# Optimization experiments

Hardware: AMD Instinct MI355X
Metric: run time of the kernel (lower is better)

## Reference

```python
import jax, jax.numpy as jnp
import numpy as np
import math

NH, NKV, D = 32, 8, 128  # heads, kv heads, head dim

def _alibi_slopes(n):
    cp2 = 2 ** math.floor(math.log2(n))
    base = 2.0 ** (-8.0 / cp2)
    slopes = base ** np.arange(1, cp2 + 1, dtype=np.float32)
    if cp2 != n:
        extra_base = 2.0 ** (-4.0 / cp2)
        extra = extra_base ** np.arange(1, 1 + 2 * (n - cp2), 2, dtype=np.float32)
        slopes = np.concatenate([slopes, extra])
    return slopes.astype(np.float32)

def setup_inputs() -> dict:
    key = jax.random.key(0)
    k1, k2, k3 = jax.random.split(key, 3)
    B, S, H = 4, 1024, 4096
    qkv_out = NH * D + 2 * NKV * D  # 6144
    return {
        "hidden_states": jax.random.normal(k1, (B, S, H), jnp.float32) * 0.02,
        "w_qkv": jax.random.normal(k2, (H, qkv_out), jnp.float32) * 0.02,
        "w_o": jax.random.normal(k3, (NH * D, H), jnp.float32) * 0.02,
    }

def reference(hidden_states, w_qkv, w_o):
    B, S, H = hidden_states.shape
    G = NH // NKV  # query groups per kv head
    scale = D ** -0.5

    qkv = hidden_states @ w_qkv  # [B,S,6144]
    q = qkv[..., : NH * D].reshape(B, S, NKV, G, D)
    k = qkv[..., NH * D : NH * D + NKV * D].reshape(B, S, NKV, D)
    v = qkv[..., NH * D + NKV * D :].reshape(B, S, NKV, D)

    scores = jnp.einsum("bqhgd,bkhd->bhgqk", q, k) * scale  # [B,NKV,G,S,S]

    slopes = jnp.asarray(_alibi_slopes(NH)).reshape(NKV, G)  # head order
    pos = jnp.arange(S)
    rel = pos[:, None] - pos[None, :]  # i - j
    sqrt_dist = jnp.sqrt(jnp.maximum(rel, 0).astype(jnp.float32))
    bias = -slopes[:, :, None, None] * sqrt_dist  # ALiBi-sqrt bias
    bias = jnp.where(rel[None, None] >= 0, bias, -jnp.inf)  # causal mask

    attn = jax.nn.softmax(scores + bias[None], axis=-1)
    out = jnp.einsum("bhgqk,bkhd->bqhgd", attn, v).reshape(B, S, NH * D)
    return out @ w_o
```

## Files before the change

kernel.cpp:

```cpp
#include <hip/hip_runtime.h>
#include <stdint.h>

typedef __attribute__((ext_vector_type(4))) float floatx4;
typedef __attribute__((ext_vector_type(8))) short short8;
typedef unsigned short ushort_t;

#define DEVI __device__ __forceinline__

constexpr int Bc   = 4;
constexpr int Sc   = 1024;
constexpr int Hc   = 4096;
constexpr int NHc  = 32;
constexpr int NKVc = 8;
constexpr int Dc   = 128;
constexpr int QKVO = 6144;
constexpr int Mc   = Bc * Sc;

DEVI ushort_t f2bf(float f) {
  union { float f; unsigned u; } x; x.f = f;
  unsigned u = x.u;
  u += 0x7fffu + ((u >> 16) & 1u);
  return (ushort_t)(u >> 16);
}

DEVI short8 cvt8(floatx4 a, floatx4 b) {
  short8 r;
  r[0] = (short)f2bf(a[0]); r[1] = (short)f2bf(a[1]);
  r[2] = (short)f2bf(a[2]); r[3] = (short)f2bf(a[3]);
  r[4] = (short)f2bf(b[0]); r[5] = (short)f2bf(b[1]);
  r[6] = (short)f2bf(b[2]); r[7] = (short)f2bf(b[3]);
  return r;
}

DEVI void load_lds16(const ushort_t* g, ushort_t* l) {
  __builtin_amdgcn_global_load_lds(
      (const __attribute__((address_space(1))) void*)g,
      (__attribute__((address_space(3))) void*)l, 16, 0, 0);
}

#define BARRIER()  asm volatile("s_barrier" ::: "memory")
#define LGKM0()    asm volatile("s_waitcnt lgkmcnt(0)" ::: "memory")
#define VMCNT(n)   asm volatile("s_waitcnt vmcnt(" #n ")" ::: "memory")

__global__ __launch_bounds__(256)
void cvt_bf16(const float* __restrict__ src, ushort_t* __restrict__ dst, int n8)
{
  const int i = blockIdx.x * 256 + threadIdx.x;
  if (i >= n8) return;
  const floatx4 f0 = *(const floatx4*)(src + (size_t)i * 8);
  const floatx4 f1 = *(const floatx4*)(src + (size_t)i * 8 + 4);
  *(short8*)(dst + (size_t)i * 8) = cvt8(f0, f1);
}

__global__ __launch_bounds__(256)
void transpose_cvt(const float* __restrict__ src, ushort_t* __restrict__ dst,
                   int R, int C)
{
  __shared__ float ts[64][67];
  const int cb = C >> 6;
  const int r0 = (blockIdx.x / cb) << 6;
  const int c0 = (blockIdx.x % cb) << 6;
  const int t  = threadIdx.x;

  const int lr = t >> 4, lc = (t & 15) << 2;
#pragma unroll
  for (int i = 0; i < 4; ++i) {
    const floatx4 v = *(const floatx4*)(src + (size_t)(r0 + lr + 16 * i) * C + c0 + lc);
#pragma unroll
    for (int j = 0; j < 4; ++j) ts[lr + 16 * i][lc + j] = v[j];
  }
  __syncthreads();

  const int c     = ((t >> 6) << 4) + ((t & 63) >> 2);
  const int chunk = t & 3;
  short8 t0, t1;
#pragma unroll
  for (int k = 0; k < 8; ++k) t0[k] = (short)f2bf(ts[chunk * 16 + k][c]);
#pragma unroll
  for (int k = 0; k < 8; ++k) t1[k] = (short)f2bf(ts[chunk * 16 + 8 + k][c]);
  ushort_t* dp = dst + (size_t)(c0 + c) * R + r0 + chunk * 16;
  *(short8*)dp       = t0;
  *(short8*)(dp + 8) = t1;
}

__global__ __launch_bounds__(256)
void v_transpose(const ushort_t* __restrict__ qkv, ushort_t* __restrict__ vt)
{
  __shared__ ushort_t ts[64][72];
  const int bid = blockIdx.x;
  const int db  = bid & 1;
  const int sb  = (bid >> 1) & 15;
  const int hkv = (bid >> 5) & 7;
  const int b   = bid >> 8;
  const int t   = threadIdx.x;

  const ushort_t* src = qkv + (size_t)(b * Sc + sb * 64) * QKVO
                        + (NHc * Dc + NKVc * Dc) + hkv * Dc + db * 64;
  const int lr = t >> 3, lc = (t & 7) * 8;
  *(short8*)&ts[lr][lc]      = *(const short8*)(src + (size_t)lr * QKVO + lc);
  *(short8*)&ts[lr + 32][lc] = *(const short8*)(src + (size_t)(lr + 32) * QKVO + lc);
  __syncthreads();

  ushort_t* dst = vt + ((size_t)(b * NKVc + hkv) * Dc + db * 64) * Sc + sb * 64;
  const int dr  = t >> 2;
  const int sc0 = (t & 3) * 16;
  short8 o0, o1;
#pragma unroll
  for (int k = 0; k < 8; ++k) o0[k] = (short)ts[sc0 + k][dr];
#pragma unroll
  for (int k = 0; k < 8; ++k) o1[k] = (short)ts[sc0 + 8 + k][dr];
  *(short8*)(dst + (size_t)dr * Sc + sc0)     = o0;
  *(short8*)(dst + (size_t)dr * Sc + sc0 + 8) = o1;
}

template<bool OBF16>
__global__ __launch_bounds__(512, 2)
void gemm_nt8(const ushort_t* __restrict__ A, const ushort_t* __restrict__ BT,
              void* __restrict__ Cp, int M, int N, int K)
{
  __shared__ __align__(16) ushort_t As[2][256 * 64];
  __shared__ __align__(16) ushort_t Bs[2][256 * 64];

  const int nb  = N >> 8;
  const int nwg = (M >> 8) * nb;
  int bid = blockIdx.x;
  bid = (bid & 7) * (nwg >> 3) + (bid >> 3);
  const int bm = bid / nb, bn = bid % nb;
  const int m0 = bm << 8, n0 = bn << 8;

  const int tid  = threadIdx.x;
  const int wid  = tid >> 6, lane = tid & 63;
  const int wm   = wid >> 2, wn = wid & 3;
  const int fr   = lane & 15;
  const int g16  = (lane >> 4) << 4;
  const int rsw  = (fr & 7) << 4;
  const int l8   = lane >> 3;
  const int scol = ((lane & 7) ^ l8) << 3;

  const int arow0 = wm * 128 + wn * 32;
  const int brow0 = (((wn >> 1) << 3) + ((wm * 2 + (wn & 1)) << 1)) * 16;

  const ushort_t* agl = A  + (size_t)(m0 + arow0 + l8) * K + scol;
  const ushort_t* bgl = BT + (size_t)(n0 + brow0 + l8) * K + scol;

  const int rowA = (wm * 128 + fr) * 128;
  const int rowB = (wn * 64 + fr) * 128;
  const int cb0  = g16 ^ rsw;
  const int cb1  = (64 + g16) ^ rsw;

  const floatx4 fz = {0.f, 0.f, 0.f, 0.f};
  floatx4 acc[8][4];
#pragma unroll
  for (int i = 0; i < 8; ++i)
#pragma unroll
    for (int f = 0; f < 4; ++f) acc[i][f] = fz;

  load_lds16(agl,                  &As[0][(arow0 +  0) * 64]);
  load_lds16(agl +  8 * (size_t)K, &As[0][(arow0 +  8) * 64]);
  load_lds16(agl + 16 * (size_t)K, &As[0][(arow0 + 16) * 64]);
  load_lds16(agl + 24 * (size_t)K, &As[0][(arow0 + 24) * 64]);
  load_lds16(bgl,                  &Bs[0][(brow0 +  0) * 64]);
  load_lds16(bgl +  8 * (size_t)K, &Bs[0][(brow0 +  8) * 64]);
  load_lds16(bgl + 16 * (size_t)K, &Bs[0][(brow0 + 16) * 64]);
  load_lds16(bgl + 24 * (size_t)K, &Bs[0][(brow0 + 24) * 64]);
  VMCNT(0);
  BARRIER();

  const int NT = K >> 6;
  for (int kt = 0; kt < NT; ++kt) {
    const int u = kt & 1, v = u ^ 1;
    const char* Au = (const char*)&As[u][0];
    const char* Bu = (const char*)&Bs[u][0];
    const bool st  = (kt + 1 < NT);
    const size_t kn = (size_t)(kt + 1) << 6;

#define LDA(i, ks) (*(const short8*)(Au + rowA + (i) * 2048 + ((ks) ? cb1 : cb0)))
#define LDB(f, ks) (*(const short8*)(Bu + rowB + (f) * 2048 + ((ks) ? cb1 : cb0)))
#define MFMA16(d, a0, a1, b0, b1)                                         \
    d = __builtin_amdgcn_mfma_f32_16x16x32_bf16(a0, b0, d, 0, 0, 0);      \
    d = __builtin_amdgcn_mfma_f32_16x16x32_bf16(a1, b1, d, 0, 0, 0);

    short8 aR[4][2], bE[2][2], bO[2][2];

#pragma unroll
    for (int i = 0; i < 4; ++i) { aR[i][0] = LDA(i, 0); aR[i][1] = LDA(i, 1); }
#pragma unroll
    for (int f = 0; f < 2; ++f) { bE[f][0] = LDB(2 * f, 0); bE[f][1] = LDB(2 * f, 1); }
    if (st) {
      load_lds16(agl + kn,                 &As[v][(arow0 + 0) * 64]);
      load_lds16(agl + 8 * (size_t)K + kn, &As[v][(arow0 + 8) * 64]);
    }
    BARRIER();
    __builtin_amdgcn_s_setprio(1);
#pragma unroll
    for (int i = 0; i < 4; ++i)
#pragma unroll
      for (int f = 0; f < 2; ++f) { MFMA16(acc[i][2 * f], aR[i][0], aR[i][1], bE[f][0], bE[f][1]); }
    __builtin_amdgcn_s_setprio(0);
    LGKM0();
    BARRIER();

#pragma unroll
    for (int i = 0; i < 4; ++i) { aR[i][0] = LDA(4 + i, 0); aR[i][1] = LDA(4 + i, 1); }
    if (st) {
      load_lds16(agl + 16 * (size_t)K + kn, &As[v][(arow0 + 16) * 64]);
      load_lds16(agl + 24 * (size_t)K + kn, &As[v][(arow0 + 24) * 64]);
    }
    BARRIER();
    __builtin_amdgcn_s_setprio(1);
#pragma unroll
    for (int i = 0; i < 4; ++i)
#pragma unroll
      for (int f = 0; f < 2; ++f) { MFMA16(acc[4 + i][2 * f], aR[i][0], aR[i][1], bE[f][0], bE[f][1]); }
    __builtin_amdgcn_s_setprio(0);
    LGKM0();
    if (st) { VMCNT(4); } else { VMCNT(0); }
    BARRIER();

#pragma unroll
    for (int f = 0; f < 2; ++f) { bO[f][0] = LDB(2 * f + 1, 0); bO[f][1] = LDB(2 * f + 1, 1); }
    if (st) {
      load_lds16(bgl + kn,                 &Bs[v][(brow0 + 0) * 64]);
      load_lds16(bgl + 8 * (size_t)K + kn, &Bs[v][(brow0 + 8) * 64]);
    }
    BARRIER();
    __builtin_amdgcn_s_setprio(1);
#pragma unroll
    for (int i = 0; i < 4; ++i)
#pragma unroll
      for (int f = 0; f < 2; ++f) { MFMA16(acc[4 + i][2 * f + 1], aR[i][0], aR[i][1], bO[f][0], bO[f][1]); }
    __builtin_amdgcn_s_setprio(0);
    LGKM0();
    BARRIER();

#pragma unroll
    for (int i = 0; i < 4; ++i) { aR[i][0] = LDA(i, 0); aR[i][1] = LDA(i, 1); }
    if (st) {
      load_lds16(bgl + 16 * (size_t)K + kn, &Bs[v][(brow0 + 16) * 64]);
      load_lds16(bgl + 24 * (size_t)K + kn, &Bs[v][(brow0 + 24) * 64]);
    }
    BARRIER();
    __builtin_amdgcn_s_setprio(1);
#pragma unroll
    for (int i = 0; i < 4; ++i)
#pragma unroll
      for (int f = 0; f < 2; ++f) { MFMA16(acc[i][2 * f + 1], aR[i][0], aR[i][1], bO[f][0], bO[f][1]); }
    __builtin_amdgcn_s_setprio(0);
    LGKM0();
    VMCNT(2);
    BARRIER();

#undef LDA
#undef LDB
#undef MFMA16
  }

  const int r4 = (lane >> 4) << 2;
#pragma unroll
  for (int i = 0; i < 8; ++i) {
#pragma unroll
    for (int rr = 0; rr < 4; ++rr) {
      const size_t row = (size_t)(m0 + wm * 128 + i * 16 + r4 + rr);
#pragma unroll
      for (int f = 0; f < 4; ++f) {
        const size_t col = (size_t)(n0 + wn * 64 + f * 16 + fr);
        if constexpr (OBF16)
          ((ushort_t*)Cp)[row * N + col] = f2bf(acc[i][f][rr]);
        else
          ((float*)Cp)[row * N + col] = acc[i][f][rr];
      }
    }
  }
}

__global__ __launch_bounds__(256, 2)
void attn_fwd(const ushort_t* __restrict__ qkv,
              const ushort_t* __restrict__ vt,
              ushort_t* __restrict__ attn)
{
  __shared__ __align__(16) ushort_t Plds[4][32 * 40];

  const int bid = blockIdx.x;
  const int x   = bid & 7;
  const int p   = bid >> 3;
  const int j   = p & 15;
  const int g   = ((p >> 4) << 3) + x;
  const int b   = g >> 3;
  const int hkv = g & 7;

  const int tid  = threadIdx.x;
  const int wid  = tid >> 6, lane = tid & 63;
  const int h    = hkv * 4 + wid;
  const int fr   = lane & 15;
  const int kk8  = (lane >> 4) << 3;
  const int q4   = (lane >> 4) << 2;
  const float slope = exp2f(-0.25f * (float)(h + 1));
  const float scale = 0.08838834764831845f;

  const ushort_t* qp  = qkv + (size_t)b * Sc * QKVO + (size_t)h * Dc;
  const ushort_t* kp  = qkv + (size_t)b * Sc * QKVO + NHc * Dc + (size_t)hkv * Dc;
  const ushort_t* vtp = vt + (size_t)(b * NKVc + hkv) * Dc * Sc;
  ushort_t* myP = &Plds[wid][0];

  const floatx4 fz = {0.f, 0.f, 0.f, 0.f};

  auto process = [&](const int qb) {
    short8 qf[2][4];
#pragma unroll
    for (int t = 0; t < 2; ++t) {
      const int qrow = qb * 32 + t * 16 + fr;
#pragma unroll
      for (int s = 0; s < 4; ++s)
        qf[t][s] = *(const short8*)(qp + (size_t)qrow * QKVO + s * 32 + kk8);
    }

    floatx4 o[2][8];
#pragma unroll
    for (int t = 0; t < 2; ++t)
#pragma unroll
      for (int jj = 0; jj < 8; ++jj) o[t][jj] = fz;
    float mrow[2][4], lrow[2][4];
#pragma unroll
    for (int t = 0; t < 2; ++t)
#pragma unroll
      for (int rr = 0; rr < 4; ++rr) { mrow[t][rr] = -1e30f; lrow[t][rr] = 0.f; }

    for (int kb = 0; kb <= qb; ++kb) {
      floatx4 s_[2][2];
      s_[0][0] = fz; s_[0][1] = fz; s_[1][0] = fz; s_[1][1] = fz;
#pragma unroll
      for (int half = 0; half < 2; ++half) {
        const int kcol = kb * 32 + half * 16 + fr;
#pragma unroll
        for (int s = 0; s < 4; ++s) {
          const short8 kf = *(const short8*)(kp + (size_t)kcol * QKVO + s * 32 + kk8);
          s_[0][half] = __builtin_amdgcn_mfma_f32_16x16x32_bf16(qf[0][s], kf, s_[0][half], 0, 0, 0);
          s_[1][half] = __builtin_amdgcn_mfma_f32_16x16x32_bf16(qf[1][s], kf, s_[1][half], 0, 0, 0);
        }
      }

      short8 vf[8];
#pragma unroll
      for (int jj = 0; jj < 8; ++jj)
        vf[jj] = *(const short8*)(vtp + (size_t)(jj * 16 + fr) * Sc + kb * 32 + kk8);

#pragma unroll
      for (int t = 0; t < 2; ++t)
#pragma unroll
        for (int rr = 0; rr < 4; ++rr) {
          const int qg  = qb * 32 + t * 16 + q4 + rr;
          const int dk0 = qg - (kb * 32 + fr);
          const int dk1 = dk0 - 16;
          s_[t][0][rr] = (dk0 >= 0)
              ? s_[t][0][rr] * scale - slope * sqrtf((float)dk0) : -1e30f;
          s_[t][1][rr] = (dk1 >= 0)
              ? s_[t][1][rr] * scale - slope * sqrtf((float)dk1) : -1e30f;
        }

      float pmv[2][4];
#pragma unroll
      for (int t = 0; t < 2; ++t)
#pragma unroll
        for (int rr = 0; rr < 4; ++rr) {
          float pm = fmaxf(s_[t][0][rr], s_[t][1][rr]);
#pragma unroll
          for (int m = 1; m < 16; m <<= 1) pm = fmaxf(pm, __shfl_xor(pm, m));
          pmv[t][rr] = pm;
        }

      int need = 0;
#pragma unroll
      for (int t = 0; t < 2; ++t)
#pragma unroll
        for (int rr = 0; rr < 4; ++rr)
          need |= (pmv[t][rr] > mrow[t][rr] + 8.f) ? 1 : 0;
      if (__any(need)) {
#pragma unroll
        for (int t = 0; t < 2; ++t)
#pragma unroll
          for (int rr = 0; rr < 4; ++rr) {
            const float mnew = fmaxf(mrow[t][rr], pmv[t][rr]);
            const float corr = __expf(mrow[t][rr] - mnew);
            lrow[t][rr] *= corr;
            mrow[t][rr] = mnew;
#pragma unroll
            for (int jj = 0; jj < 8; ++jj) o[t][jj][rr] *= corr;
          }
      }

#pragma unroll
      for (int t = 0; t < 2; ++t)
#pragma unroll
        for (int rr = 0; rr < 4; ++rr) {
          const float p0 = __expf(s_[t][0][rr] - mrow[t][rr]);
          const float p1 = __expf(s_[t][1][rr] - mrow[t][rr]);
          lrow[t][rr] += p0 + p1;
          myP[(t * 16 + q4 + rr) * 40 + fr]      = f2bf(p0);
          myP[(t * 16 + q4 + rr) * 40 + 16 + fr] = f2bf(p1);
        }
      short8 pa[2];
      pa[0] = *(const short8*)&myP[fr * 40 + kk8];
      pa[1] = *(const short8*)&myP[(16 + fr) * 40 + kk8];

#pragma unroll
      for (int jj = 0; jj < 8; ++jj) {
        o[0][jj] = __builtin_amdgcn_mfma_f32_16x16x32_bf16(pa[0], vf[jj], o[0][jj], 0, 0, 0);
        o[1][jj] = __builtin_amdgcn_mfma_f32_16x16x32_bf16(pa[1], vf[jj], o[1][jj], 0, 0, 0);
      }
    }

#pragma unroll
    for (int t = 0; t < 2; ++t)
#pragma unroll
      for (int rr = 0; rr < 4; ++rr) {
        float rs = lrow[t][rr];
#pragma unroll
        for (int m = 1; m < 16; m <<= 1) rs += __shfl_xor(rs, m);
        const float inv = 1.f / rs;
        const size_t tok = (size_t)b * Sc + qb * 32 + t * 16 + q4 + rr;
#pragma unroll
        for (int jj = 0; jj < 8; ++jj)
          attn[tok * (size_t)(NHc * Dc) + h * Dc + jj * 16 + fr] = f2bf(o[t][jj][rr] * inv);
      }
  };

  process(31 - j);
  process(j);
}

extern "C" void kernel_launch(void* const* d_in, const int* in_sizes, int n_in,
                              void* d_out, int out_size, void* d_ws, size_t ws_size,
                              hipStream_t stream)
{
  const float* hidden = (const float*)d_in[0];
  const float* w_qkv  = (const float*)d_in[1];
  const float* w_o    = (const float*)d_in[2];
  float* out = (float*)d_out;

  ushort_t* wqT   = (ushort_t*)d_ws;
  ushort_t* hidb  = wqT + (size_t)QKVO * Hc;
  ushort_t* qkvb  = hidb + (size_t)Mc * Hc;
  ushort_t* attnb = hidb;
  ushort_t* woT   = wqT;
  ushort_t* vtb   = wqT + (size_t)Mc * Hc;

  cvt_bf16<<<dim3((Mc * Hc / 8) / 256), dim3(256), 0, stream>>>(
      hidden, hidb, Mc * Hc / 8);
  transpose_cvt<<<dim3((Hc / 64) * (QKVO / 64)), dim3(256), 0, stream>>>(
      w_qkv, wqT, Hc, QKVO);
  gemm_nt8<true><<<dim3((Mc / 256) * (QKVO / 256)), dim3(512), 0, stream>>>(
      hidb, wqT, qkvb, Mc, QKVO, Hc);
  v_transpose<<<dim3(1024), dim3(256), 0, stream>>>(qkvb, vtb);
  attn_fwd<<<dim3(512), dim3(256), 0, stream>>>(qkvb, vtb, attnb);
  transpose_cvt<<<dim3((Hc / 64) * (Hc / 64)), dim3(256), 0, stream>>>(
      w_o, woT, Hc, Hc);
  gemm_nt8<false><<<dim3((Mc / 256) * (Hc / 256)), dim3(512), 0, stream>>>(
      attnb, woT, out, Mc, Hc, Hc);
}
```

Before: 576.8 us.

## Issue all next-tile global-to-LDS loads up front and keep A fragments in registers

The GEMM main loop now issues all eight global-to-LDS loads for the next K tile at once, right after the first fragment reads, instead of spreading them across four phases. Staggered vmcnt waits gate each phase on the data it needs. Separate low and high A register sets (aL/aH) remove the fourth A reload from LDS, and the explicit lgkmcnt waits are dropped. It also remaps which rows each wave loads. The trade-offs are more registers in use, and the vmcnt counting must line up exactly with the in-order completion of loads into the LDS regions being read.

```diff
diff --git a/kernel.cpp b/kernel.cpp
--- a/kernel.cpp
+++ b/kernel.cpp
@@ -39,7 +39,6 @@
 }
 
 #define BARRIER()  asm volatile("s_barrier" ::: "memory")
-#define LGKM0()    asm volatile("s_waitcnt lgkmcnt(0)" ::: "memory")
 #define VMCNT(n)   asm volatile("s_waitcnt vmcnt(" #n ")" ::: "memory")
 
 __global__ __launch_bounds__(256)
@@ -137,11 +136,12 @@
   const int l8   = lane >> 3;
   const int scol = ((lane & 7) ^ l8) << 3;
 
-  const int arow0 = wm * 128 + wn * 32;
-  const int brow0 = (((wn >> 1) << 3) + ((wm * 2 + (wn & 1)) << 1)) * 16;
-
-  const ushort_t* agl = A  + (size_t)(m0 + arow0 + l8) * K + scol;
-  const ushort_t* bgl = BT + (size_t)(n0 + brow0 + l8) * K + scol;
+  const int abase = ((wid >> 2) << 7) + ((wid & 3) << 4);
+  const int bbase = wid << 5;
+
+  const size_t Ks = (size_t)K;
+  const ushort_t* ag = A  + (size_t)(m0 + abase + l8) * K + scol;
+  const ushort_t* bg = BT + (size_t)(n0 + bbase + l8) * K + scol;
 
   const int rowA = (wm * 128 + fr) * 128;
   const int rowB = (wn * 64 + fr) * 128;
@@ -155,15 +155,19 @@
 #pragma unroll
     for (int f = 0; f < 4; ++f) acc[i][f] = fz;
 
-  load_lds16(agl,                  &As[0][(arow0 +  0) * 64]);
-  load_lds16(agl +  8 * (size_t)K, &As[0][(arow0 +  8) * 64]);
-  load_lds16(agl + 16 * (size_t)K, &As[0][(arow0 + 16) * 64]);
-  load_lds16(agl + 24 * (size_t)K, &As[0][(arow0 + 24) * 64]);
-  load_lds16(bgl,                  &Bs[0][(brow0 +  0) * 64]);
-  load_lds16(bgl +  8 * (size_t)K, &Bs[0][(brow0 +  8) * 64]);
-  load_lds16(bgl + 16 * (size_t)K, &Bs[0][(brow0 + 16) * 64]);
-  load_lds16(bgl + 24 * (size_t)K, &Bs[0][(brow0 + 24) * 64]);
-  VMCNT(0);
+  auto STAGE = [&](int v, size_t kn) {
+    load_lds16(ag + kn,            &As[v][(abase +  0) * 64]);
+    load_lds16(ag +  8 * Ks + kn,  &As[v][(abase +  8) * 64]);
+    load_lds16(bg + kn,            &Bs[v][(bbase +  0) * 64]);
+    load_lds16(bg +  8 * Ks + kn,  &Bs[v][(bbase +  8) * 64]);
+    load_lds16(ag + 64 * Ks + kn,  &As[v][(abase + 64) * 64]);
+    load_lds16(ag + 72 * Ks + kn,  &As[v][(abase + 72) * 64]);
+    load_lds16(bg + 16 * Ks + kn,  &Bs[v][(bbase + 16) * 64]);
+    load_lds16(bg + 24 * Ks + kn,  &Bs[v][(bbase + 24) * 64]);
+  };
+
+  STAGE(0, 0);
+  VMCNT(4);
   BARRIER();
 
   const int NT = K >> 6;
@@ -172,7 +176,6 @@
     const char* Au = (const char*)&As[u][0];
     const char* Bu = (const char*)&Bs[u][0];
     const bool st  = (kt + 1 < NT);
-    const size_t kn = (size_t)(kt + 1) << 6;
 
 #define LDA(i, ks) (*(const short8*)(Au + rowA + (i) * 2048 + ((ks) ? cb1 : cb0)))
 #define LDB(f, ks) (*(const short8*)(Bu + rowB + (f) * 2048 + ((ks) ? cb1 : cb0)))
@@ -180,74 +183,53 @@
     d = __builtin_amdgcn_mfma_f32_16x16x32_bf16(a0, b0, d, 0, 0, 0);      \
     d = __builtin_amdgcn_mfma_f32_16x16x32_bf16(a1, b1, d, 0, 0, 0);
 
-    short8 aR[4][2], bE[2][2], bO[2][2];
-
-#pragma unroll
-    for (int i = 0; i < 4; ++i) { aR[i][0] = LDA(i, 0); aR[i][1] = LDA(i, 1); }
+    short8 aL[4][2], aH[4][2], bE[2][2], bO[2][2];
+
+#pragma unroll
+    for (int i = 0; i < 4; ++i) { aL[i][0] = LDA(i, 0); aL[i][1] = LDA(i, 1); }
 #pragma unroll
     for (int f = 0; f < 2; ++f) { bE[f][0] = LDB(2 * f, 0); bE[f][1] = LDB(2 * f, 1); }
-    if (st) {
-      load_lds16(agl + kn,                 &As[v][(arow0 + 0) * 64]);
-      load_lds16(agl + 8 * (size_t)K + kn, &As[v][(arow0 + 8) * 64]);
-    }
+    if (st) STAGE(v, (size_t)(kt + 1) << 6);
     BARRIER();
     __builtin_amdgcn_s_setprio(1);
 #pragma unroll
     for (int i = 0; i < 4; ++i)
 #pragma unroll
-      for (int f = 0; f < 2; ++f) { MFMA16(acc[i][2 * f], aR[i][0], aR[i][1], bE[f][0], bE[f][1]); }
+      for (int f = 0; f < 2; ++f) { MFMA16(acc[i][2 * f], aL[i][0], aL[i][1], bE[f][0], bE[f][1]); }
     __builtin_amdgcn_s_setprio(0);
-    LGKM0();
-    BARRIER();
-
-#pragma unroll
-    for (int i = 0; i < 4; ++i) { aR[i][0] = LDA(4 + i, 0); aR[i][1] = LDA(4 + i, 1); }
-    if (st) {
-      load_lds16(agl + 16 * (size_t)K + kn, &As[v][(arow0 + 16) * 64]);
-      load_lds16(agl + 24 * (size_t)K + kn, &As[v][(arow0 + 24) * 64]);
-    }
+    if (st) { VMCNT(10); } else { VMCNT(2); }
+    BARRIER();
+
+#pragma unroll
+    for (int i = 0; i < 4; ++i) { aH[i][0] = LDA(4 + i, 0); aH[i][1] = LDA(4 + i, 1); }
     BARRIER();
     __builtin_amdgcn_s_setprio(1);
 #pragma unroll
     for (int i = 0; i < 4; ++i)
 #pragma unroll
-      for (int f = 0; f < 2; ++f) { MFMA16(acc[4 + i][2 * f], aR[i][0], aR[i][1], bE[f][0], bE[f][1]); }
+      for (int f = 0; f < 2; ++f) { MFMA16(acc[4 + i][2 * f], aH[i][0], aH[i][1], bE[f][0], bE[f][1]); }
     __builtin_amdgcn_s_setprio(0);
-    LGKM0();
-    if (st) { VMCNT(4); } else { VMCNT(0); }
+    if (st) { VMCNT(8); } else { VMCNT(0); }
     BARRIER();
 
 #pragma unroll
     for (int f = 0; f < 2; ++f) { bO[f][0] = LDB(2 * f + 1, 0); bO[f][1] = LDB(2 * f + 1, 1); }
-    if (st) {
-      load_lds16(bgl + kn,                 &Bs[v][(brow0 + 0) * 64]);
-      load_lds16(bgl + 8 * (size_t)K + kn, &Bs[v][(brow0 + 8) * 64]);
-    }
     BARRIER();
     __builtin_amdgcn_s_setprio(1);
 #pragma unroll
     for (int i = 0; i < 4; ++i)
 #pragma unroll
-      for (int f = 0; f < 2; ++f) { MFMA16(acc[4 + i][2 * f + 1], aR[i][0], aR[i][1], bO[f][0], bO[f][1]); }
+      for (int f = 0; f < 2; ++f) { MFMA16(acc[4 + i][2 * f + 1], aH[i][0], aH[i][1], bO[f][0], bO[f][1]); }
     __builtin_amdgcn_s_setprio(0);
-    LGKM0();
-    BARRIER();
-
-#pragma unroll
-    for (int i = 0; i < 4; ++i) { aR[i][0] = LDA(i, 0); aR[i][1] = LDA(i, 1); }
-    if (st) {
-      load_lds16(bgl + 16 * (size_t)K + kn, &Bs[v][(brow0 + 16) * 64]);
-      load_lds16(bgl + 24 * (size_t)K + kn, &Bs[v][(brow0 + 24) * 64]);
-    }
-    BARRIER();
+    BARRIER();
+
     __builtin_amdgcn_s_setprio(1);
 #pragma unroll
     for (int i = 0; i < 4; ++i)
 #pragma unroll
-      for (int f = 0; f < 2; ++f) { MFMA16(acc[i][2 * f + 1], aR[i][0], aR[i][1], bO[f][0], bO[f][1]); }
+      for (int f = 0; f < 2; ++f) { MFMA16(acc[i][2 * f + 1], aL[i][0], aL[i][1], bO[f][0], bO[f][1]); }
     __builtin_amdgcn_s_setprio(0);
-    LGKM0();
-    VMCNT(2);
+    if (st) { VMCNT(4); }
     BARRIER();
 
 #undef LDA
```

Result: no change. 578.9 us (+0.4%).
